# Kernel optimization log

Hardware: AMD Instinct MI355X
Metric: run time of the kernel (lower is better)

The kernel has to match this reference:

```python
import jax, jax.numpy as jnp
import numpy as np

T = 8192
F = 128   # feature_size
H = 2048  # hidden_size
PRED_LEN = 12  # pred_length (fc_out head exists in module but is unused in forward)


def setup_inputs() -> dict:
    key = jax.random.key(0)
    ks = jax.random.split(key, 10)
    s_ih = 1.0 / np.sqrt(H)
    inp = {
        "x": jax.random.normal(ks[0], (T, F), dtype=jnp.float32),
        # PyTorch nn.LSTM params, gate order [i, f, g, o]
        "W_ih": jax.random.uniform(ks[1], (4 * H, F), jnp.float32, -s_ih, s_ih),
        "W_hh": jax.random.uniform(ks[2], (4 * H, H), jnp.float32, -s_ih, s_ih),
        "b_ih": jax.random.uniform(ks[3], (4 * H,), jnp.float32, -s_ih, s_ih),
        "b_hh": jax.random.uniform(ks[4], (4 * H,), jnp.float32, -s_ih, s_ih),
        # self.linear: Linear(H, H)
        "W_lin": jax.random.uniform(ks[5], (H, H), jnp.float32, -s_ih, s_ih),
        "b_lin": jax.random.uniform(ks[6], (H,), jnp.float32, -s_ih, s_ih),
        # self.one_out: Linear(H, 2)
        "W_out": jax.random.uniform(ks[7], (2, H), jnp.float32, -s_ih, s_ih),
        "b_out": jax.random.uniform(ks[8], (2,), jnp.float32, -s_ih, s_ih),
    }
    return inp


def _lstm_last_h(x, W_ih, W_hh, b_ih, b_hh):
    # x: [T, F]; returns final hidden state h: [H]
    # Precompute input projections for all timesteps: [T, 4H]
    x_proj = x @ W_ih.T + (b_ih + b_hh)

    def step(carry, xp):
        h, c = carry
        gates = xp + h @ W_hh.T  # [4H]
        i = jax.nn.sigmoid(gates[0 * H:1 * H])
        f = jax.nn.sigmoid(gates[1 * H:2 * H])
        g = jnp.tanh(gates[2 * H:3 * H])
        o = jax.nn.sigmoid(gates[3 * H:4 * H])
        c = f * c + i * g
        h = o * jnp.tanh(c)
        return (h, c), None

    h0 = jnp.zeros((H,), x.dtype)
    c0 = jnp.zeros((H,), x.dtype)
    (h, _), _ = jax.lax.scan(step, (h0, c0), x_proj)
    return h


def reference(x, W_ih, W_hh, b_ih, b_hh, W_lin, b_lin, W_out, b_out):
    h = _lstm_last_h(x, W_ih, W_hh, b_ih, b_hh)        # [H]
    y = h @ W_lin.T + b_lin                            # [H]
    y = y @ W_out.T + b_out                            # [2]
    return y.reshape(1, 1, 2)                          # matches torch (1,1,2)
```

## Files before the change

kernel.cpp:

```cpp
#include <hip/hip_runtime.h>


#define H      2048
#define TSTEPS 8192
#define FEAT   128
#define NBLK   256
#define NTHR   512

typedef float vf4 __attribute__((ext_vector_type(4)));
typedef float vf2 __attribute__((ext_vector_type(2)));
typedef unsigned long long u64;
typedef unsigned int u32;

__device__ __forceinline__ float sigm(float xv) {
  return __builtin_amdgcn_rcpf(1.0f + __expf(-xv));
}
__device__ __forceinline__ float tanh_(float xv) {
  return 1.0f - 2.0f * __builtin_amdgcn_rcpf(__expf(2.0f * xv) + 1.0f);
}

__device__ __forceinline__ u64 aload64(const u64* p) {
  return __hip_atomic_load(p, __ATOMIC_RELAXED, __HIP_MEMORY_SCOPE_AGENT);
}
__device__ __forceinline__ u32 aload32(const u32* p) {
  return __hip_atomic_load(p, __ATOMIC_RELAXED, __HIP_MEMORY_SCOPE_AGENT);
}
__device__ __forceinline__ void astoref(float* p, float v) {
  __hip_atomic_store(p, v, __ATOMIC_RELAXED, __HIP_MEMORY_SCOPE_AGENT);
}
__device__ __forceinline__ void astoreu(u32* p, u32 v) {
  __hip_atomic_store(p, v, __ATOMIC_RELAXED, __HIP_MEMORY_SCOPE_AGENT);
}

#define DECLG(g) vf4 w##g##_0, w##g##_1, w##g##_2, w##g##_3, \
                     w##g##_4, w##g##_5, w##g##_6, w##g##_7; \
                 vf2 wih##g; float bias##g; float acc##g;

#define LOADG(g) { \
  const int row_ = (g) * H + j; \
  const float* wr_ = W_hh + (long)row_ * H; \
  w##g##_0 = *(const vf4*)(wr_ + 4*(ln      )); \
  w##g##_1 = *(const vf4*)(wr_ + 4*(ln +  64)); \
  w##g##_2 = *(const vf4*)(wr_ + 4*(ln + 128)); \
  w##g##_3 = *(const vf4*)(wr_ + 4*(ln + 192)); \
  w##g##_4 = *(const vf4*)(wr_ + 4*(ln + 256)); \
  w##g##_5 = *(const vf4*)(wr_ + 4*(ln + 320)); \
  w##g##_6 = *(const vf4*)(wr_ + 4*(ln + 384)); \
  w##g##_7 = *(const vf4*)(wr_ + 4*(ln + 448)); \
  wih##g  = *(const vf2*)(W_ih + (long)row_ * FEAT + 2*ln); \
  bias##g = b_ih[row_] + b_hh[row_]; }

#define PIN(g) asm volatile("" : \
  "+v"(w##g##_0), "+v"(w##g##_1), "+v"(w##g##_2), "+v"(w##g##_3), \
  "+v"(w##g##_4), "+v"(w##g##_5), "+v"(w##g##_6), "+v"(w##g##_7), \
  "+v"(wih##g), "+v"(bias##g));

#define LDSREAD(k, ldsrow) \
  const vf4 hv##k = *(const vf4*)&(ldsrow)[4*(ln + 64*(k))];

#define FMA_G(g, c) \
  acc##g = __builtin_fmaf(w##g##_##c.x, h4_.x, acc##g); \
  acc##g = __builtin_fmaf(w##g##_##c.y, h4_.y, acc##g); \
  acc##g = __builtin_fmaf(w##g##_##c.z, h4_.z, acc##g); \
  acc##g = __builtin_fmaf(w##g##_##c.w, h4_.w, acc##g);

#define FMA_C(c) { const vf4 h4_ = hv##c; \
  FMA_G(0, c) FMA_G(1, c) FMA_G(2, c) FMA_G(3, c) }

#define REDUCE(g) { float a_ = acc##g; \
  a_ += __shfl_xor(a_, 1);  a_ += __shfl_xor(a_, 2);  a_ += __shfl_xor(a_, 4); \
  a_ += __shfl_xor(a_, 8);  a_ += __shfl_xor(a_, 16); a_ += __shfl_xor(a_, 32); \
  acc##g = a_ + bias##g; }

__device__ __forceinline__ void poll_and_stage(const u32* __restrict__ slots,
                                               const float* __restrict__ hsrc,
                                               int tgt,
                                               float* __restrict__ ldsrow,
                                               int wv, int ln) {
  const u32* sp = slots + wv * 32 + (ln & 31);
  int v = (int)aload32(sp);
  while (!__all((ln < 32) ? (v >= tgt) : 1)) {
    __builtin_amdgcn_s_sleep(1);
    if ((ln < 32) && (v < tgt)) v = (int)aload32(sp);
  }
  const int base = wv * 256 + 4 * ln;
  const u64* hp = (const u64*)(hsrc + base);
  const u64 d0 = aload64(hp);
  const u64 d1 = aload64(hp + 1);
  vf4 hv;
  hv.x = __uint_as_float((u32)d0);
  hv.y = __uint_as_float((u32)(d0 >> 32));
  hv.z = __uint_as_float((u32)d1);
  hv.w = __uint_as_float((u32)(d1 >> 32));
  *(vf4*)&ldsrow[base] = hv;
}

__global__ __launch_bounds__(NTHR, 2)
void lstm_persist(const float* __restrict__ x,
                  const float* __restrict__ W_ih,
                  const float* __restrict__ W_hh,
                  const float* __restrict__ b_ih,
                  const float* __restrict__ b_hh,
                  const float* __restrict__ W_lin,
                  const float* __restrict__ b_lin,
                  const float* __restrict__ W_out,
                  const float* __restrict__ b_out,
                  float* __restrict__ out,
                  float* __restrict__ ws)
{
  const int tid = threadIdx.x;
  const int b   = blockIdx.x;
  const int wv  = tid >> 6;
  const int ln  = tid & 63;

  float* hbuf0 = ws;
  float* hbuf1 = ws + H;
  u32*   slots = (u32*)(ws + 2 * H);

  __shared__ __align__(16) float h_lds[2][H];

  *(vf4*)&h_lds[0][4 * tid] = (vf4)(0.0f);

  const int j = b * 8 + wv;
  DECLG(0) DECLG(1) DECLG(2) DECLG(3)
  LOADG(0) LOADG(1) LOADG(2) LOADG(3)
  PIN(0) PIN(1) PIN(2) PIN(3)

  __syncthreads();

  float cst = 0.0f;

  #pragma unroll 1
  for (int t = 0; t < TSTEPS; ++t) {
    const vf2 xr = *(const vf2*)(x + (long)t * FEAT + 2 * ln);
    float* ldsrow = h_lds[t & 1];

    if (t > 0)
      poll_and_stage(slots, (t & 1) ? hbuf1 : hbuf0, t, ldsrow, wv, ln);
    __syncthreads();

    LDSREAD(0, ldsrow) LDSREAD(1, ldsrow) LDSREAD(2, ldsrow) LDSREAD(3, ldsrow)
    LDSREAD(4, ldsrow) LDSREAD(5, ldsrow) LDSREAD(6, ldsrow) LDSREAD(7, ldsrow)

    acc0 = wih0.x * xr.x + wih0.y * xr.y;
    acc1 = wih1.x * xr.x + wih1.y * xr.y;
    acc2 = wih2.x * xr.x + wih2.y * xr.y;
    acc3 = wih3.x * xr.x + wih3.y * xr.y;

    FMA_C(0) FMA_C(1) FMA_C(2) FMA_C(3)
    FMA_C(4) FMA_C(5) FMA_C(6) FMA_C(7)

    REDUCE(0) REDUCE(1) REDUCE(2) REDUCE(3)

    const float iv = sigm(acc0);
    const float fv = sigm(acc1);
    const float gv = tanh_(acc2);
    const float ov = sigm(acc3);
    cst = fv * cst + iv * gv;
    const float hval = ov * tanh_(cst);

    if (ln == 0)
      astoref((((t + 1) & 1) ? hbuf1 : hbuf0) + j, hval);

    __syncthreads();
    if (tid == 0)
      astoreu(slots + b, (u32)(t + 1));
  }

  {
    float* ldsrow = h_lds[0];
    poll_and_stage(slots, hbuf0, TSTEPS, ldsrow, wv, ln);
    __syncthreads();

    float a0 = 0.0f;
    const float* wl = W_lin + (long)j * H;
    #pragma unroll
    for (int k = 0; k < 8; ++k) {
      const vf4 h4 = *(const vf4*)&ldsrow[4 * (ln + 64 * k)];
      const vf4 u  = *(const vf4*)(wl + 4 * (ln + 64 * k));
      a0 += u.x * h4.x + u.y * h4.y + u.z * h4.z + u.w * h4.w;
    }
    a0 += __shfl_xor(a0, 1);  a0 += __shfl_xor(a0, 2);  a0 += __shfl_xor(a0, 4);
    a0 += __shfl_xor(a0, 8);  a0 += __shfl_xor(a0, 16); a0 += __shfl_xor(a0, 32);

    if (ln == 0)
      astoref(hbuf1 + j, a0 + b_lin[j]);
    __syncthreads();
    if (tid == 0)
      astoreu(slots + b, (u32)(TSTEPS + 1));
  }

  if (b == 0 && wv == 0) {
    const u32* sp = slots + 4 * ln;
    int v0 = (int)aload32(sp + 0), v1 = (int)aload32(sp + 1);
    int v2 = (int)aload32(sp + 2), v3 = (int)aload32(sp + 3);
    const int tgt = TSTEPS + 1;
    while (!__all((v0 >= tgt) & (v1 >= tgt) & (v2 >= tgt) & (v3 >= tgt))) {
      __builtin_amdgcn_s_sleep(1);
      if (v0 < tgt) v0 = (int)aload32(sp + 0);
      if (v1 < tgt) v1 = (int)aload32(sp + 1);
      if (v2 < tgt) v2 = (int)aload32(sp + 2);
      if (v3 < tgt) v3 = (int)aload32(sp + 3);
    }
    float p0 = 0.0f, p1 = 0.0f;
    #pragma unroll
    for (int k = 0; k < 16; ++k) {
      const u64 d  = aload64((const u64*)hbuf1 + ln + 64 * k);
      const int c  = 2 * (ln + 64 * k);
      const float ylo = __uint_as_float((u32)d);
      const float yhi = __uint_as_float((u32)(d >> 32));
      p0 = __builtin_fmaf(W_out[c],         ylo, p0);
      p0 = __builtin_fmaf(W_out[c + 1],     yhi, p0);
      p1 = __builtin_fmaf(W_out[H + c],     ylo, p1);
      p1 = __builtin_fmaf(W_out[H + c + 1], yhi, p1);
    }
    p0 += __shfl_xor(p0, 1);  p0 += __shfl_xor(p0, 2);  p0 += __shfl_xor(p0, 4);
    p0 += __shfl_xor(p0, 8);  p0 += __shfl_xor(p0, 16); p0 += __shfl_xor(p0, 32);
    p1 += __shfl_xor(p1, 1);  p1 += __shfl_xor(p1, 2);  p1 += __shfl_xor(p1, 4);
    p1 += __shfl_xor(p1, 8);  p1 += __shfl_xor(p1, 16); p1 += __shfl_xor(p1, 32);
    if (ln == 0) {
      out[0] = p0 + b_out[0];
      out[1] = p1 + b_out[1];
    }
  }
}

extern "C" void kernel_launch(void* const* d_in, const int* in_sizes, int n_in,
                              void* d_out, int out_size, void* d_ws, size_t ws_size,
                              hipStream_t stream) {
  const float* x     = (const float*)d_in[0];
  const float* W_ih  = (const float*)d_in[1];
  const float* W_hh  = (const float*)d_in[2];
  const float* b_ih  = (const float*)d_in[3];
  const float* b_hh  = (const float*)d_in[4];
  const float* W_lin = (const float*)d_in[5];
  const float* b_lin = (const float*)d_in[6];
  const float* W_out = (const float*)d_in[7];
  const float* b_out = (const float*)d_in[8];

  lstm_persist<<<dim3(NBLK), dim3(NTHR), 0, stream>>>(
      x, W_ih, W_hh, b_ih, b_hh, W_lin, b_lin, W_out, b_out,
      (float*)d_out, (float*)d_ws);
}
```

Before: 34.44 ms.

## Replace per-step block barriers with per-wave LDS flags and counter-based publish

Result: slower. 50.43 ms (+46.4%).

```diff
diff --git a/kernel.cpp b/kernel.cpp
--- a/kernel.cpp
+++ b/kernel.cpp
@@ -72,28 +72,10 @@
   a_ += __shfl_xor(a_, 8);  a_ += __shfl_xor(a_, 16); a_ += __shfl_xor(a_, 32); \
   acc##g = a_ + bias##g; }
 
-__device__ __forceinline__ void poll_and_stage(const u32* __restrict__ slots,
-                                               const float* __restrict__ hsrc,
-                                               int tgt,
-                                               float* __restrict__ ldsrow,
-                                               int wv, int ln) {
-  const u32* sp = slots + wv * 32 + (ln & 31);
-  int v = (int)aload32(sp);
-  while (!__all((ln < 32) ? (v >= tgt) : 1)) {
-    __builtin_amdgcn_s_sleep(1);
-    if ((ln < 32) && (v < tgt)) v = (int)aload32(sp);
-  }
-  const int base = wv * 256 + 4 * ln;
-  const u64* hp = (const u64*)(hsrc + base);
-  const u64 d0 = aload64(hp);
-  const u64 d1 = aload64(hp + 1);
-  vf4 hv;
-  hv.x = __uint_as_float((u32)d0);
-  hv.y = __uint_as_float((u32)(d0 >> 32));
-  hv.z = __uint_as_float((u32)d1);
-  hv.w = __uint_as_float((u32)(d1 >> 32));
-  *(vf4*)&ldsrow[base] = hv;
-}
+#define SPIN(s) \
+  while (__hip_atomic_load(&flag[s], __ATOMIC_ACQUIRE, \
+                           __HIP_MEMORY_SCOPE_WORKGROUP) < t) {} \
+  asm volatile("" ::: "memory");
 
 __global__ __launch_bounds__(NTHR, 2)
 void lstm_persist(const float* __restrict__ x,
@@ -118,8 +100,12 @@
   u32*   slots = (u32*)(ws + 2 * H);
 
   __shared__ __align__(16) float h_lds[2][H];
+  __shared__ int flag[8];
+  __shared__ int pub_cnt;
 
   *(vf4*)&h_lds[0][4 * tid] = (vf4)(0.0f);
+  if (tid < 8) flag[tid] = 0;
+  if (tid == 0) pub_cnt = 0;
 
   const int j = b * 8 + wv;
   DECLG(0) DECLG(1) DECLG(2) DECLG(3)
@@ -135,20 +121,43 @@
     const vf2 xr = *(const vf2*)(x + (long)t * FEAT + 2 * ln);
     float* ldsrow = h_lds[t & 1];
 
-    if (t > 0)
-      poll_and_stage(slots, (t & 1) ? hbuf1 : hbuf0, t, ldsrow, wv, ln);
-    __syncthreads();
-
-    LDSREAD(0, ldsrow) LDSREAD(1, ldsrow) LDSREAD(2, ldsrow) LDSREAD(3, ldsrow)
-    LDSREAD(4, ldsrow) LDSREAD(5, ldsrow) LDSREAD(6, ldsrow) LDSREAD(7, ldsrow)
+    if (t > 0) {
+      const u32* sp = slots + wv * 32 + (ln & 31);
+      int v = (ln < 32) ? (int)aload32(sp) : 0x7fffffff;
+      while (!__all(v >= t)) {
+        __builtin_amdgcn_s_sleep(1);
+        if ((ln < 32) && (v < t)) v = (int)aload32(sp);
+      }
+      const int base = wv * 256 + 4 * ln;
+      const float* hsrc = (t & 1) ? hbuf1 : hbuf0;
+      const u64* hp = (const u64*)(hsrc + base);
+      const u64 d0 = aload64(hp);
+      const u64 d1 = aload64(hp + 1);
+      vf4 hv;
+      hv.x = __uint_as_float((u32)d0);
+      hv.y = __uint_as_float((u32)(d0 >> 32));
+      hv.z = __uint_as_float((u32)d1);
+      hv.w = __uint_as_float((u32)(d1 >> 32));
+      *(vf4*)&ldsrow[base] = hv;
+      if (ln == 0)
+        __hip_atomic_store(&flag[wv], t, __ATOMIC_RELEASE,
+                           __HIP_MEMORY_SCOPE_WORKGROUP);
+      asm volatile("" ::: "memory");
+    }
 
     acc0 = wih0.x * xr.x + wih0.y * xr.y;
     acc1 = wih1.x * xr.x + wih1.y * xr.y;
     acc2 = wih2.x * xr.x + wih2.y * xr.y;
     acc3 = wih3.x * xr.x + wih3.y * xr.y;
 
-    FMA_C(0) FMA_C(1) FMA_C(2) FMA_C(3)
-    FMA_C(4) FMA_C(5) FMA_C(6) FMA_C(7)
+    SPIN(0) LDSREAD(0, ldsrow) FMA_C(0)
+    SPIN(1) LDSREAD(1, ldsrow) FMA_C(1)
+    SPIN(2) LDSREAD(2, ldsrow) FMA_C(2)
+    SPIN(3) LDSREAD(3, ldsrow) FMA_C(3)
+    SPIN(4) LDSREAD(4, ldsrow) FMA_C(4)
+    SPIN(5) LDSREAD(5, ldsrow) FMA_C(5)
+    SPIN(6) LDSREAD(6, ldsrow) FMA_C(6)
+    SPIN(7) LDSREAD(7, ldsrow) FMA_C(7)
 
     REDUCE(0) REDUCE(1) REDUCE(2) REDUCE(3)
 
@@ -161,15 +170,32 @@
 
     if (ln == 0)
       astoref((((t + 1) & 1) ? hbuf1 : hbuf0) + j, hval);
-
-    __syncthreads();
-    if (tid == 0)
-      astoreu(slots + b, (u32)(t + 1));
+    asm volatile("s_waitcnt vmcnt(0)" ::: "memory");
+    if (ln == 0) {
+      const int old = atomicAdd(&pub_cnt, 1);
+      if (old == 8 * t + 7)
+        astoreu(slots + b, (u32)(t + 1));
+    }
   }
 
   {
     float* ldsrow = h_lds[0];
-    poll_and_stage(slots, hbuf0, TSTEPS, ldsrow, wv, ln);
+    const u32* sp = slots + wv * 32 + (ln & 31);
+    int v = (ln < 32) ? (int)aload32(sp) : 0x7fffffff;
+    while (!__all(v >= TSTEPS)) {
+      __builtin_amdgcn_s_sleep(1);
+      if ((ln < 32) && (v < TSTEPS)) v = (int)aload32(sp);
+    }
+    const int base = wv * 256 + 4 * ln;
+    const u64* hp = (const u64*)(hbuf0 + base);
+    const u64 d0 = aload64(hp);
+    const u64 d1 = aload64(hp + 1);
+    vf4 hv;
+    hv.x = __uint_as_float((u32)d0);
+    hv.y = __uint_as_float((u32)(d0 >> 32));
+    hv.z = __uint_as_float((u32)d1);
+    hv.w = __uint_as_float((u32)(d1 >> 32));
+    *(vf4*)&ldsrow[base] = hv;
     __syncthreads();
 
     float a0 = 0.0f;
```
